# Performance work log

Hardware: AMD Instinct MI355X
Metric: run time of the kernel (lower is better)

## Reference

```python
import jax, jax.numpy as jnp
import numpy as np


def setup_inputs() -> dict:
    key = jax.random.key(0)
    k1, k2, k3 = jax.random.split(key, 3)
    B, C, H, W = 32, 192, 64, 64
    L = 64  # number of unique quantization levels in the sos codebook
    x = jax.random.normal(k1, (B, C, H, W), dtype=jnp.float32) * 4.0
    means = jax.random.normal(k2, (B, C, H, W), dtype=jnp.float32)
    # sorted 1-D codebook of unique quantizer levels (sos.unique_values)
    codebook = jnp.sort(jax.random.normal(k3, (L,), dtype=jnp.float32) * 4.0)
    return {"x": x, "means": means, "codebook": codebook}


def _nearest_level(r, codebook):
    """Vectorized version of transform_map: for each element of r, the index of
    the nearest codebook value (argmin |codebook - r|), using searchsorted on
    the sorted codebook instead of a dense [N, L] distance matrix."""
    L = codebook.shape[0]
    pos = jnp.clip(jnp.searchsorted(codebook, r), 1, L - 1)  # right neighbor
    left = codebook[pos - 1]
    right = codebook[pos]
    return jnp.where(r - left <= right - r, pos - 1, pos)  # int32 symbols


def reference(x, means, codebook):
    # quantize(mode='symbols'): subtract means, map each value to the index of
    # the nearest codebook level (the map_sos_cdf dict lookup / argmin loop).
    r = x - means
    symbols = _nearest_level(r, codebook)          # [B,C,H,W] int32
    # dequantize: map symbols back to float levels (map_cdf_sos) and add means.
    y_hat = jnp.take(codebook, symbols) + means    # [B,C,H,W] float32
    return symbols, y_hat
```

## Files before the change

### kernel.cpp

```cpp
#include <hip/hip_runtime.h>
#include <math.h>


#define NCELL 1024

typedef float f32x4 __attribute__((ext_vector_type(4)));

__device__ __forceinline__ int cellof(float v, float lo, float scale) {
    float t = (v - lo) * scale;
    t = fminf(fmaxf(t, 0.0f), (float)(NCELL - 1));
    return (int)t;
}

__global__ __launch_bounds__(256) void quant_dequant_kernel(
    const float4* __restrict__ x4,
    const float4* __restrict__ m4,
    const float*  __restrict__ codebook,
    f32x4* __restrict__ sym_out,
    f32x4* __restrict__ yhat_out,
    int n4)
{
    __shared__ float s_cb[64];
    __shared__ float s_mid[64];
    __shared__ unsigned short s_fm[64];
    __shared__ unsigned short s_lut[NCELL];

    const int tid = threadIdx.x;
    if (tid < 64) s_cb[tid] = codebook[tid];
    __syncthreads();
    if (tid < 64)
        s_mid[tid] = (tid < 63) ? 0.5f * (s_cb[tid] + s_cb[tid + 1])
                                : INFINITY;
    const float lo    = s_cb[0];
    const float hi    = s_cb[63];
    const float range = hi - lo;
    const float scale = (range > 0.0f) ? ((float)NCELL / range) : 0.0f;
    __syncthreads();
    if (tid < 64)
        s_fm[tid] = (tid < 63) ? (unsigned short)cellof(s_mid[tid], lo, scale)
                               : (unsigned short)0xFFFF;
    __syncthreads();

#pragma unroll
    for (int e = 0; e < NCELL / 256; ++e) {
        const int c = tid + e * 256;
        int pos = 0;
#pragma unroll
        for (int s = 32; s > 0; s >>= 1)
            pos += (s_fm[pos + s - 1] < c) ? s : 0;
        s_lut[c] = (unsigned short)pos;
    }
    __syncthreads();

    const int stride = gridDim.x * blockDim.x;
    int i = blockIdx.x * blockDim.x + tid;

    for (; i + 3 * stride < n4; i += 4 * stride) {
        float4 xv[4], mv[4];
#pragma unroll
        for (int u = 0; u < 4; ++u) {
            xv[u] = x4[i + u * stride];
            mv[u] = m4[i + u * stride];
        }
#pragma unroll
        for (int u = 0; u < 4; ++u) {
            float rr[4] = { xv[u].x - mv[u].x, xv[u].y - mv[u].y,
                            xv[u].z - mv[u].z, xv[u].w - mv[u].w };
            float mm[4] = { mv[u].x, mv[u].y, mv[u].z, mv[u].w };
            f32x4 sy, yh;
#pragma unroll
            for (int k = 0; k < 4; ++k) {
                const float r = rr[k];
                const int idx = cellof(r, lo, scale);
                int pos = (int)s_lut[idx];
                while (s_mid[pos] < r) ++pos;
                sy[k] = (float)pos;
                yh[k] = s_cb[pos] + mm[k];
            }
            __builtin_nontemporal_store(sy, &sym_out[i + u * stride]);
            __builtin_nontemporal_store(yh, &yhat_out[i + u * stride]);
        }
    }
    for (; i < n4; i += stride) {
        const float4 xv = x4[i];
        const float4 mv = m4[i];
        float rr[4] = { xv.x - mv.x, xv.y - mv.y, xv.z - mv.z, xv.w - mv.w };
        float mm[4] = { mv.x, mv.y, mv.z, mv.w };
        f32x4 sy, yh;
#pragma unroll
        for (int k = 0; k < 4; ++k) {
            const float r = rr[k];
            const int idx = cellof(r, lo, scale);
            int pos = (int)s_lut[idx];
            while (s_mid[pos] < r) ++pos;
            sy[k] = (float)pos;
            yh[k] = s_cb[pos] + mm[k];
        }
        __builtin_nontemporal_store(sy, &sym_out[i]);
        __builtin_nontemporal_store(yh, &yhat_out[i]);
    }
}

extern "C" void kernel_launch(void* const* d_in, const int* in_sizes, int n_in,
                              void* d_out, int out_size, void* d_ws, size_t ws_size,
                              hipStream_t stream)
{
    const float* x     = (const float*)d_in[0];
    const float* means = (const float*)d_in[1];
    const float* cb    = (const float*)d_in[2];

    const int n  = in_sizes[0];
    const int n4 = n / 4;

    float* out = (float*)d_out;

    const int block = 256;
    const int grid  = 2048;

    quant_dequant_kernel<<<grid, block, 0, stream>>>(
        (const float4*)x, (const float4*)means, cb,
        (f32x4*)out, (f32x4*)(out + n), n4);
}
```

Baseline: 353.5 us.

## Precompute LUT in separate kernel, bound search width, software-pipeline loads

Moves LUT and midpoint construction into a single-block pre-kernel that writes to workspace and also computes the maximum number of levels per cell. The main kernel copies the precomputed tables into shared memory, replaces the data-dependent while loop with a fixed-width branchless count (a fast path when the width is at most 2), and prefetches the next iteration's loads in a double-buffered loop. It also drops nontemporal stores. This removes the per-block LUT build and the divergent search loop, but adds a second launch and uses plain stores, which may pollute the cache.

```diff
diff --git a/kernel.cpp b/kernel.cpp
--- a/kernel.cpp
+++ b/kernel.cpp
@@ -3,8 +3,6 @@
 
 
 #define NCELL 1024
-
-typedef float f32x4 __attribute__((ext_vector_type(4)));
 
 __device__ __forceinline__ int cellof(float v, float lo, float scale) {
     float t = (v - lo) * scale;
@@ -12,35 +10,33 @@
     return (int)t;
 }
 
-__global__ __launch_bounds__(256) void quant_dequant_kernel(
-    const float4* __restrict__ x4,
-    const float4* __restrict__ m4,
-    const float*  __restrict__ codebook,
-    f32x4* __restrict__ sym_out,
-    f32x4* __restrict__ yhat_out,
-    int n4)
+__global__ __launch_bounds__(256) void build_lut_kernel(
+    const float* __restrict__ codebook,
+    float* __restrict__ ws_mid,
+    unsigned short* __restrict__ ws_lut,
+    unsigned int* __restrict__ ws_w)
 {
     __shared__ float s_cb[64];
-    __shared__ float s_mid[64];
     __shared__ unsigned short s_fm[64];
-    __shared__ unsigned short s_lut[NCELL];
+    __shared__ unsigned int s_lut32[NCELL / 2];
+    __shared__ unsigned int s_red[4];
+    unsigned short* s_lut = (unsigned short*)s_lut32;
 
     const int tid = threadIdx.x;
     if (tid < 64) s_cb[tid] = codebook[tid];
     __syncthreads();
-    if (tid < 64)
-        s_mid[tid] = (tid < 63) ? 0.5f * (s_cb[tid] + s_cb[tid + 1])
-                                : INFINITY;
     const float lo    = s_cb[0];
-    const float hi    = s_cb[63];
-    const float range = hi - lo;
+    const float range = s_cb[63] - lo;
     const float scale = (range > 0.0f) ? ((float)NCELL / range) : 0.0f;
-    __syncthreads();
-    if (tid < 64)
-        s_fm[tid] = (tid < 63) ? (unsigned short)cellof(s_mid[tid], lo, scale)
+    if (tid < 64) {
+        float mid = (tid < 63) ? 0.5f * (s_cb[tid] + s_cb[tid + 1]) : INFINITY;
+        ws_mid[tid] = mid;
+        s_fm[tid] = (tid < 63) ? (unsigned short)cellof(mid, lo, scale)
                                : (unsigned short)0xFFFF;
+    }
     __syncthreads();
 
+    unsigned short myl[NCELL / 256];
 #pragma unroll
     for (int e = 0; e < NCELL / 256; ++e) {
         const int c = tid + e * 256;
@@ -48,56 +44,128 @@
 #pragma unroll
         for (int s = 32; s > 0; s >>= 1)
             pos += (s_fm[pos + s - 1] < c) ? s : 0;
+        myl[e] = (unsigned short)pos;
         s_lut[c] = (unsigned short)pos;
     }
     __syncthreads();
 
-    const int stride = gridDim.x * blockDim.x;
-    int i = blockIdx.x * blockDim.x + tid;
+    unsigned int mymax = 0;
+#pragma unroll
+    for (int e = 0; e < NCELL / 256; ++e) {
+        const int c = tid + e * 256;
+        unsigned int nxt = (c == NCELL - 1) ? 63u : (unsigned int)s_lut[c + 1];
+        mymax = max(mymax, nxt - (unsigned int)myl[e]);
+        ws_lut[c] = myl[e];
+    }
+#pragma unroll
+    for (int off = 32; off > 0; off >>= 1)
+        mymax = max(mymax, (unsigned int)__shfl_down((int)mymax, off));
+    if ((tid & 63) == 0) s_red[tid >> 6] = mymax;
+    __syncthreads();
+    if (tid == 0) {
+        unsigned int w = max(max(s_red[0], s_red[1]), max(s_red[2], s_red[3]));
+        *ws_w = (w < 1u) ? 1u : w;
+    }
+}
 
-    for (; i + 3 * stride < n4; i += 4 * stride) {
-        float4 xv[4], mv[4];
-#pragma unroll
-        for (int u = 0; u < 4; ++u) {
-            xv[u] = x4[i + u * stride];
-            mv[u] = m4[i + u * stride];
-        }
-#pragma unroll
-        for (int u = 0; u < 4; ++u) {
-            float rr[4] = { xv[u].x - mv[u].x, xv[u].y - mv[u].y,
-                            xv[u].z - mv[u].z, xv[u].w - mv[u].w };
-            float mm[4] = { mv[u].x, mv[u].y, mv[u].z, mv[u].w };
-            f32x4 sy, yh;
-#pragma unroll
-            for (int k = 0; k < 4; ++k) {
-                const float r = rr[k];
-                const int idx = cellof(r, lo, scale);
-                int pos = (int)s_lut[idx];
-                while (s_mid[pos] < r) ++pos;
-                sy[k] = (float)pos;
-                yh[k] = s_cb[pos] + mm[k];
-            }
-            __builtin_nontemporal_store(sy, &sym_out[i + u * stride]);
-            __builtin_nontemporal_store(yh, &yhat_out[i + u * stride]);
-        }
-    }
-    for (; i < n4; i += stride) {
-        const float4 xv = x4[i];
-        const float4 mv = m4[i];
-        float rr[4] = { xv.x - mv.x, xv.y - mv.y, xv.z - mv.z, xv.w - mv.w };
-        float mm[4] = { mv.x, mv.y, mv.z, mv.w };
-        f32x4 sy, yh;
+__device__ __forceinline__ void process4(
+    const float4 xv, const float4 mv,
+    const float lo, const float scale, const int W,
+    const float* s_cb, const float* s_mid, const unsigned short* s_lut,
+    float4& sy, float4& yh)
+{
+    float rr[4] = { xv.x - mv.x, xv.y - mv.y, xv.z - mv.z, xv.w - mv.w };
+    float mm[4] = { mv.x, mv.y, mv.z, mv.w };
+    float sv[4], yv[4];
+    if (W <= 2) {
 #pragma unroll
         for (int k = 0; k < 4; ++k) {
             const float r = rr[k];
-            const int idx = cellof(r, lo, scale);
-            int pos = (int)s_lut[idx];
-            while (s_mid[pos] < r) ++pos;
-            sy[k] = (float)pos;
-            yh[k] = s_cb[pos] + mm[k];
+            const int start = (int)s_lut[cellof(r, lo, scale)];
+            const int pos = start + ((s_mid[start] < r) ? 1 : 0)
+                                  + ((s_mid[start + 1] < r) ? 1 : 0);
+            sv[k] = (float)pos;
+            yv[k] = s_cb[pos] + mm[k];
         }
-        __builtin_nontemporal_store(sy, &sym_out[i]);
-        __builtin_nontemporal_store(yh, &yhat_out[i]);
+    } else {
+#pragma unroll
+        for (int k = 0; k < 4; ++k) {
+            const float r = rr[k];
+            const int start = (int)s_lut[cellof(r, lo, scale)];
+            int pos = start;
+            for (int j = 0; j < W; ++j)
+                pos += (s_mid[start + j] < r) ? 1 : 0;
+            sv[k] = (float)pos;
+            yv[k] = s_cb[pos] + mm[k];
+        }
+    }
+    sy = make_float4(sv[0], sv[1], sv[2], sv[3]);
+    yh = make_float4(yv[0], yv[1], yv[2], yv[3]);
+}
+
+__global__ __launch_bounds__(256) void quant_dequant_kernel(
+    const float4* __restrict__ x4,
+    const float4* __restrict__ m4,
+    const float*  __restrict__ codebook,
+    const float*  __restrict__ ws_mid,
+    const unsigned int* __restrict__ ws_lut32,
+    const unsigned int* __restrict__ ws_w,
+    float4* __restrict__ sym_out,
+    float4* __restrict__ yhat_out,
+    int n4)
+{
+    __shared__ float s_cb[64];
+    __shared__ float s_mid[128];
+    __shared__ unsigned int s_lut32[NCELL / 2];
+    __shared__ unsigned int s_wv;
+    const unsigned short* s_lut = (const unsigned short*)s_lut32;
+
+    const int tid = threadIdx.x;
+    if (tid < 64)  s_cb[tid]  = codebook[tid];
+    if (tid < 128) s_mid[tid] = (tid < 64) ? ws_mid[tid] : INFINITY;
+    s_lut32[tid]       = ws_lut32[tid];
+    s_lut32[tid + 256] = ws_lut32[tid + 256];
+    if (tid == 0) s_wv = *ws_w;
+    __syncthreads();
+
+    const float lo    = s_cb[0];
+    const float range = s_cb[63] - lo;
+    const float scale = (range > 0.0f) ? ((float)NCELL / range) : 0.0f;
+    const int   W     = (int)s_wv;
+
+    const int stride = gridDim.x * blockDim.x;
+    const int step   = 2 * stride;
+    const int n4_main = n4 - (n4 % step);
+
+    int base = blockIdx.x * blockDim.x + tid;
+    if (base < n4_main) {
+        float4 ax0 = x4[base], ax1 = x4[base + stride];
+        float4 am0 = m4[base], am1 = m4[base + stride];
+        int nb = base + step;
+        while (true) {
+            float4 bx0, bx1, bm0, bm1;
+            const bool more = (nb < n4_main);
+            if (more) {
+                bx0 = x4[nb]; bx1 = x4[nb + stride];
+                bm0 = m4[nb]; bm1 = m4[nb + stride];
+            }
+            float4 sy0, yh0, sy1, yh1;
+            process4(ax0, am0, lo, scale, W, s_cb, s_mid, s_lut, sy0, yh0);
+            process4(ax1, am1, lo, scale, W, s_cb, s_mid, s_lut, sy1, yh1);
+            sym_out[base]           = sy0;
+            yhat_out[base]          = yh0;
+            sym_out[base + stride]  = sy1;
+            yhat_out[base + stride] = yh1;
+            if (!more) break;
+            ax0 = bx0; ax1 = bx1; am0 = bm0; am1 = bm1;
+            base = nb; nb += step;
+        }
+    }
+    for (int i = n4_main + blockIdx.x * blockDim.x + tid; i < n4; i += stride) {
+        float4 sy, yh;
+        process4(x4[i], m4[i], lo, scale, W, s_cb, s_mid, s_lut, sy, yh);
+        sym_out[i]  = sy;
+        yhat_out[i] = yh;
     }
 }
 
@@ -114,10 +182,16 @@
 
     float* out = (float*)d_out;
 
+    float*          ws_mid = (float*)d_ws;
+    unsigned short* ws_lut = (unsigned short*)((char*)d_ws + 256);
+    unsigned int*   ws_w   = (unsigned int*)((char*)d_ws + 256 + 2048);
+
+    build_lut_kernel<<<1, 256, 0, stream>>>(cb, ws_mid, ws_lut, ws_w);
+
     const int block = 256;
     const int grid  = 2048;
-
     quant_dequant_kernel<<<grid, block, 0, stream>>>(
         (const float4*)x, (const float4*)means, cb,
-        (f32x4*)out, (f32x4*)(out + n), n4);
+        ws_mid, (const unsigned int*)ws_lut, ws_w,
+        (float4*)out, (float4*)(out + n), n4);
 }
```

New measurement: 346.3 us. 2.1% less time.
